# Kernel optimization log

Hardware: AMD Instinct MI355X
Metric: run time of the kernel (lower is better)

## Reference

```python
import jax, jax.numpy as jnp
import numpy as np

BUCKET_SIZE = 512
# Classic perfect-spatial-hashing primes (PSH / Teschner et al.)
P1 = np.uint32(73856093)
P2 = np.uint32(19349663)
P3 = np.uint32(83492791)
P4 = np.uint32(2654435761)  # mixes batch id into the hash


def setup_inputs() -> dict:
    key = jax.random.key(0)
    k1, k2 = jax.random.split(key)
    N, B = 4_000_000, 16
    coords = jax.random.normal(k1, (N, 3), dtype=jnp.float32) * 10.0
    seps = jnp.sort(jax.random.randint(k2, (B,), 0, N, dtype=jnp.int32))
    return {"coords": coords, "seps": seps, "hash_op": 1}


def reference(coords, seps, hash_op):
    """Hash-based bucket scatter with padding (PSHScatterLayer forward).

    Each point is voxelized, spatially hashed (mixed with its batch id from
    `seps`) into one of num_buckets buckets; points are written into a padded
    [pad_to, 3] buffer at slot = bucket * BUCKET_SIZE + within-bucket rank.
    Points overflowing a bucket are dropped (finite-capacity bucket counter).
    Deterministic rank (arrival order) replaces the CUDA atomic counter.
    """
    N = coords.shape[0]
    pad_to = ((N + BUCKET_SIZE - 1) // BUCKET_SIZE) * BUCKET_SIZE
    num_buckets = pad_to // BUCKET_SIZE

    # voxelize + spatial hash (non-differentiable index path)
    vox = jnp.floor(jax.lax.stop_gradient(coords)).astype(jnp.int32).astype(jnp.uint32)  # [N,3]
    batch_id = jnp.searchsorted(seps, jnp.arange(N, dtype=seps.dtype), side='right').astype(jnp.uint32)
    h = (vox[:, 0] * P1) ^ (vox[:, 1] * P2) ^ (vox[:, 2] * P3) ^ (batch_id * P4)
    h = h + jnp.uint32(hash_op)
    bucket = (h % jnp.uint32(num_buckets)).astype(jnp.int32)  # [N]

    # per-bucket counts and within-bucket rank (stable order = arrival order)
    counts = jax.ops.segment_sum(jnp.ones((N,), jnp.int32), bucket, num_segments=num_buckets)
    starts = jnp.cumsum(counts) - counts                      # [num_buckets]
    order = jnp.argsort(bucket)                               # stable in jax
    rank_sorted = jnp.arange(N, dtype=jnp.int32) - starts[bucket[order]]
    rank = jnp.zeros((N,), jnp.int32).at[order].set(rank_sorted)

    slot = bucket * BUCKET_SIZE + rank
    idx = jnp.where(rank < BUCKET_SIZE, slot, pad_to)         # out-of-range -> dropped
    scattered_coord = jnp.zeros((pad_to, 3), coords.dtype).at[idx].set(coords, mode='drop')
    return scattered_coord, counts, bucket
```

## Files before the change

### kernel.cpp

```cpp
#include <hip/hip_runtime.h>
#include <stdint.h>

#define PR1 73856093u
#define PR2 19349663u
#define PR3 83492791u
#define PR4 2654435761u
#define GS  32
#define PPT 4
#define BBITS 13

__device__ __forceinline__ uint32_t fastmod(uint32_t h, uint32_t d, double inv) {
    uint32_t q = (uint32_t)((double)h * inv);
    int32_t r = (int32_t)(h - q * d);
    if (r >= (int32_t)d) r -= d;
    if (r < 0) r += d;
    return (uint32_t)r;
}

__global__ void k_bucket_hist(const float* __restrict__ coords,
                              const int* __restrict__ seps, int B,
                              const int* __restrict__ hash_op_p,
                              int N, int NB, int chunk, double invNB,
                              float* __restrict__ out_bucket,
                              int* __restrict__ chunk_hist) {
    extern __shared__ int hist[];
    __shared__ int s_seps[1024];
    const int tid = threadIdx.x;
    for (int i = tid; i < NB; i += blockDim.x) hist[i] = 0;
    const int Bc = B < 1024 ? B : 1024;
    for (int j = tid; j < Bc; j += blockDim.x) s_seps[j] = seps[j];
    __syncthreads();

    const uint32_t hop = (uint32_t)hash_op_p[0];
    const int start = blockIdx.x * chunk;
    const int end   = min(start + chunk, N);
    int bid = 0;
    for (int i = start + tid; i < end; i += blockDim.x) {
        while (bid < B) {
            const int sv = (bid < 1024) ? s_seps[bid] : seps[bid];
            if (sv <= i) bid++; else break;
        }
        const float x = coords[3 * (size_t)i + 0];
        const float y = coords[3 * (size_t)i + 1];
        const float z = coords[3 * (size_t)i + 2];
        const uint32_t vx = (uint32_t)(int32_t)floorf(x);
        const uint32_t vy = (uint32_t)(int32_t)floorf(y);
        const uint32_t vz = (uint32_t)(int32_t)floorf(z);
        uint32_t h = vx * PR1 ^ vy * PR2 ^ vz * PR3 ^ ((uint32_t)bid * PR4);
        h += hop;
        const uint32_t b = fastmod(h, (uint32_t)NB, invNB);
        out_bucket[i] = (float)b;
        atomicAdd(&hist[(int)b], 1);
    }
    __syncthreads();
    int* dst = chunk_hist + (size_t)blockIdx.x * NB;
    for (int i = tid; i < NB; i += blockDim.x) dst[i] = hist[i];
}

__global__ void k_scan_group(int* __restrict__ ch, int* __restrict__ Sg,
                             int C, int NB) {
    const int b = blockIdx.x * blockDim.x + threadIdx.x;
    if (b >= NB) return;
    const int g  = blockIdx.y;
    const int c0 = g * GS;
    const int c1 = min(c0 + GS, C);
    int run = 0;
    for (int c = c0; c < c1; c++) {
        const size_t idx = (size_t)c * NB + b;
        const int v = ch[idx];
        ch[idx] = run;
        run += v;
    }
    Sg[(size_t)g * NB + b] = run;
}

__global__ void k_scan_tops(int* __restrict__ Sg, int G, int NB,
                            float* __restrict__ out_counts,
                            float* __restrict__ out_sc) {
    const int b = blockIdx.x * blockDim.x + threadIdx.x;
    if (b >= NB) return;
    int run = 0;
    for (int g = 0; g < G; g++) {
        const size_t idx = (size_t)g * NB + b;
        const int v = Sg[idx];
        Sg[idx] = run;
        run += v;
    }
    out_counts[b] = (float)run;
    const int c0 = run < 512 ? run : 512;
    float* p = out_sc + ((size_t)b * 512 + c0) * 3;
    for (int j = c0; j < 512; j++) {
        p[0] = 0.f; p[1] = 0.f; p[2] = 0.f;
        p += 3;
    }
}

__global__ __launch_bounds__(256, 4)
void k_scatter(const float* __restrict__ coords,
               const float* __restrict__ bucket_f,
               const int* __restrict__ ch,
               const int* __restrict__ Sg,
               int N, int NB, int chunk,
               float* __restrict__ out_sc) {
    extern __shared__ int hist[];
    const int tid = threadIdx.x;
    const int c = blockIdx.x;
    const int g = c / GS;
    const int* r1 = ch + (size_t)c * NB;
    const int* r2 = Sg + (size_t)g * NB;
    for (int i = tid; i < NB; i += blockDim.x) hist[i] = r1[i] + r2[i];
    __syncthreads();

    const int start = c * chunk;
    const int end   = min(start + chunk, N);
    const int len   = end > start ? end - start : 0;
    const int per_round = (int)blockDim.x * PPT;
    const int rounds = (len + per_round - 1) / per_round;
    const int lane = tid & 63;
    const int wv   = tid >> 6;
    const int nw   = (int)blockDim.x >> 6;
    const unsigned long long ltmask = ((unsigned long long)1 << lane) - 1;

    for (int rd = 0; rd < rounds; rd++) {
        const int wbase = start + rd * per_round + wv * (64 * PPT);
        int bs[PPT], leader[PPT], cntv[PPT], rnk[PPT];
        float cx[PPT], cy[PPT], cz[PPT];

        #pragma unroll
        for (int s = 0; s < PPT; s++) {
            const int i = wbase + s * 64 + lane;
            const bool v = (i < end);
            bs[s] = v ? (int)bucket_f[i] : NB;
            cx[s] = v ? coords[3 * (size_t)i + 0] : 0.f;
            cy[s] = v ? coords[3 * (size_t)i + 1] : 0.f;
            cz[s] = v ? coords[3 * (size_t)i + 2] : 0.f;
        }

        #pragma unroll
        for (int s = 0; s < PPT; s++) {
            const int b = bs[s];
            unsigned long long mm = ~0ull;
            #pragma unroll
            for (int k = 0; k < BBITS; k++) {
                const unsigned long long blt = __ballot(((b >> k) & 1) != 0);
                mm &= ((b >> k) & 1) ? blt : ~blt;
            }
            leader[s] = (int)__builtin_ctzll(mm);
            cntv[s]   = (int)__builtin_popcountll(mm);
            rnk[s]    = (int)__builtin_popcountll(mm & ltmask);
        }

        int basev[PPT];
        for (int w = 0; w < nw; w++) {
            if (wv == w) {
                #pragma unroll
                for (int s = 0; s < PPT; s++) {
                    int old = 0;
                    if (bs[s] < NB && lane == leader[s])
                        old = atomicAdd(&hist[bs[s]], cntv[s]);
                    basev[s] = __shfl(old, leader[s], 64);
                }
            }
            __syncthreads();
        }

        #pragma unroll
        for (int s = 0; s < PPT; s++) {
            if (bs[s] < NB) {
                const int r = basev[s] + rnk[s];
                if (r < 512) {
                    float* p = out_sc + ((size_t)bs[s] * 512 + r) * 3;
                    p[0] = cx[s]; p[1] = cy[s]; p[2] = cz[s];
                }
            }
        }
    }
}

extern "C" void kernel_launch(void* const* d_in, const int* in_sizes, int n_in,
                              void* d_out, int out_size, void* d_ws, size_t ws_size,
                              hipStream_t stream) {
    const float* coords  = (const float*)d_in[0];
    const int*   seps    = (const int*)d_in[1];
    const int*   hash_op = (const int*)d_in[2];

    const int N = in_sizes[0] / 3;
    const int B = in_sizes[1];
    const int pad_to = ((N + 511) / 512) * 512;
    const int NB = pad_to / 512;

    float* out        = (float*)d_out;
    float* out_counts = out + (size_t)pad_to * 3;
    float* out_bucket = out_counts + NB;

    const size_t rowbytes = (size_t)NB * sizeof(int);
    const long rows = (long)(ws_size / rowbytes);
    int C = 1024;
    while (C > 1 && (long)(C + (C + GS - 1) / GS) > rows) C--;
    if (C < 1) C = 1;
    const int G = (C + GS - 1) / GS;
    const int chunk = (N + C - 1) / C;
    int* chunk_hist = (int*)d_ws;
    int* Sg = chunk_hist + (size_t)C * NB;
    const size_t lds = rowbytes;
    const double invNB = 1.0 / (double)NB;

    k_bucket_hist<<<C, 256, lds, stream>>>(coords, seps, B, hash_op, N, NB, chunk,
                                           invNB, out_bucket, chunk_hist);
    dim3 g2a((NB + 255) / 256, G);
    k_scan_group<<<g2a, 256, 0, stream>>>(chunk_hist, Sg, C, NB);
    k_scan_tops<<<(NB + 255) / 256, 256, 0, stream>>>(Sg, G, NB, out_counts, out);
    k_scatter<<<C, 256, lds, stream>>>(coords, out_bucket, chunk_hist, Sg,
                                       N, NB, chunk, out);
}
```

Measured before the change: 225.3 us.

## Store per-chunk bucket histograms as uint16 and remap block-to-chunk order across XCDs

Per-chunk histogram rows shrink from int32 to uint16, which roughly halves the workspace traffic written by the histogram kernel and read by the scan and scatter kernels. Group-local prefixes are clamped to 512 so they fit in 16 bits. Because a bucket's group prefix can already exceed 512, the clamped offset still lands the point at rank 512 or above and it is dropped. Block indices are also remapped so consecutive chunks go to blocks spread across the 8 dispatch partitions, and the workspace sizing loop now steps C down in multiples of 8 to keep that remap valid.

```diff
diff --git a/kernel.cpp b/kernel.cpp
--- a/kernel.cpp
+++ b/kernel.cpp
@@ -17,12 +17,16 @@
     return (uint32_t)r;
 }
 
+__device__ __forceinline__ int chunk_of(int bi, int C) {
+    return ((C & 7) == 0) ? ((bi & 7) * (C >> 3) + (bi >> 3)) : bi;
+}
+
 __global__ void k_bucket_hist(const float* __restrict__ coords,
                               const int* __restrict__ seps, int B,
                               const int* __restrict__ hash_op_p,
-                              int N, int NB, int chunk, double invNB,
+                              int N, int NB, int C, int chunk, double invNB,
                               float* __restrict__ out_bucket,
-                              int* __restrict__ chunk_hist) {
+                              uint16_t* __restrict__ ch) {
     extern __shared__ int hist[];
     __shared__ int s_seps[1024];
     const int tid = threadIdx.x;
@@ -32,7 +36,8 @@
     __syncthreads();
 
     const uint32_t hop = (uint32_t)hash_op_p[0];
-    const int start = blockIdx.x * chunk;
+    const int c = chunk_of(blockIdx.x, C);
+    const int start = c * chunk;
     const int end   = min(start + chunk, N);
     int bid = 0;
     for (int i = start + tid; i < end; i += blockDim.x) {
@@ -53,11 +58,11 @@
         atomicAdd(&hist[(int)b], 1);
     }
     __syncthreads();
-    int* dst = chunk_hist + (size_t)blockIdx.x * NB;
-    for (int i = tid; i < NB; i += blockDim.x) dst[i] = hist[i];
-}
-
-__global__ void k_scan_group(int* __restrict__ ch, int* __restrict__ Sg,
+    uint16_t* dst = ch + (size_t)c * NB;
+    for (int i = tid; i < NB; i += blockDim.x) dst[i] = (uint16_t)hist[i];
+}
+
+__global__ void k_scan_group(uint16_t* __restrict__ ch, int* __restrict__ Sg,
                              int C, int NB) {
     const int b = blockIdx.x * blockDim.x + threadIdx.x;
     if (b >= NB) return;
@@ -68,7 +73,7 @@
     for (int c = c0; c < c1; c++) {
         const size_t idx = (size_t)c * NB + b;
         const int v = ch[idx];
-        ch[idx] = run;
+        ch[idx] = (uint16_t)(run < 512 ? run : 512);
         run += v;
     }
     Sg[(size_t)g * NB + b] = run;
@@ -98,17 +103,17 @@
 __global__ __launch_bounds__(256, 4)
 void k_scatter(const float* __restrict__ coords,
                const float* __restrict__ bucket_f,
-               const int* __restrict__ ch,
+               const uint16_t* __restrict__ ch,
                const int* __restrict__ Sg,
-               int N, int NB, int chunk,
+               int N, int NB, int C, int chunk,
                float* __restrict__ out_sc) {
     extern __shared__ int hist[];
     const int tid = threadIdx.x;
-    const int c = blockIdx.x;
+    const int c = chunk_of(blockIdx.x, C);
     const int g = c / GS;
-    const int* r1 = ch + (size_t)c * NB;
-    const int* r2 = Sg + (size_t)g * NB;
-    for (int i = tid; i < NB; i += blockDim.x) hist[i] = r1[i] + r2[i];
+    const uint16_t* r1 = ch + (size_t)c * NB;
+    const int*      r2 = Sg + (size_t)g * NB;
+    for (int i = tid; i < NB; i += blockDim.x) hist[i] = (int)r1[i] + r2[i];
     __syncthreads();
 
     const int start = c * chunk;
@@ -193,23 +198,24 @@
     float* out_counts = out + (size_t)pad_to * 3;
     float* out_bucket = out_counts + NB;
 
-    const size_t rowbytes = (size_t)NB * sizeof(int);
-    const long rows = (long)(ws_size / rowbytes);
     int C = 1024;
-    while (C > 1 && (long)(C + (C + GS - 1) / GS) > rows) C--;
-    if (C < 1) C = 1;
+    while (C > 8) {
+        const int G_ = (C + GS - 1) / GS;
+        if ((size_t)C * NB * 2 + (size_t)G_ * NB * 4 <= ws_size) break;
+        C -= 8;
+    }
     const int G = (C + GS - 1) / GS;
     const int chunk = (N + C - 1) / C;
-    int* chunk_hist = (int*)d_ws;
-    int* Sg = chunk_hist + (size_t)C * NB;
-    const size_t lds = rowbytes;
+    uint16_t* ch = (uint16_t*)d_ws;
+    int* Sg = (int*)((char*)d_ws + (((size_t)C * NB * 2 + 15) & ~(size_t)15));
+    const size_t lds = (size_t)NB * sizeof(int);
     const double invNB = 1.0 / (double)NB;
 
-    k_bucket_hist<<<C, 256, lds, stream>>>(coords, seps, B, hash_op, N, NB, chunk,
-                                           invNB, out_bucket, chunk_hist);
+    k_bucket_hist<<<C, 256, lds, stream>>>(coords, seps, B, hash_op, N, NB, C,
+                                           chunk, invNB, out_bucket, ch);
     dim3 g2a((NB + 255) / 256, G);
-    k_scan_group<<<g2a, 256, 0, stream>>>(chunk_hist, Sg, C, NB);
+    k_scan_group<<<g2a, 256, 0, stream>>>(ch, Sg, C, NB);
     k_scan_tops<<<(NB + 255) / 256, 256, 0, stream>>>(Sg, G, NB, out_counts, out);
-    k_scatter<<<C, 256, lds, stream>>>(coords, out_bucket, chunk_hist, Sg,
-                                       N, NB, chunk, out);
-}
+    k_scatter<<<C, 256, lds, stream>>>(coords, out_bucket, ch, Sg,
+                                       N, NB, C, chunk, out);
+}
```

After: 217.4 us. -3.5%, faster.
